# Kernel tuning notes

Hardware: AMD Instinct MI355X
Metric: run time of the kernel (lower is better)

The kernel has to match this reference:

```python
import jax, jax.numpy as jnp
import numpy as np

EPS = 1e-5
NUM_HEADS = 8


def _conv(x, w, pad, dil=1, groups=1, b=None):
    y = jax.lax.conv_general_dilated(
        x, w, (1, 1), pad, rhs_dilation=(dil, dil),
        dimension_numbers=('NCHW', 'OIHW', 'NCHW'), feature_group_count=groups)
    if b is not None:
        y = y + b[None, :, None, None]
    return y


def _bn_relu(x, gamma, beta):
    # BatchNorm2d in training mode: batch statistics over (N,H,W) per channel
    mu = x.mean(axis=(0, 2, 3), keepdims=True)
    var = x.var(axis=(0, 2, 3), keepdims=True)
    y = (x - mu) / jnp.sqrt(var + EPS) * gamma[None, :, None, None] + beta[None, :, None, None]
    return jax.nn.relu(y)


def _ln(x, w, b):
    # WithBias LayerNorm over channel dim (to_3d makes C the last axis)
    mu = x.mean(axis=1, keepdims=True)
    var = x.var(axis=1, keepdims=True)
    return (x - mu) / jnp.sqrt(var + EPS) * w[None, :, None, None] + b[None, :, None, None]


def _l2n(t):
    # torch F.normalize: x / max(||x||_2, 1e-12)
    return t / jnp.maximum(jnp.linalg.norm(t, axis=-1, keepdims=True), 1e-12)


def _forward(x, ln_w, ln_b, wd1, gd1, bd1, wd2, gd2, bd2, wd3, gd3, bd3,
             w_out1, w1, b1, w2, b2, w3, b3, w4, b4, w5, b5, w6, b6, w_out2):
    B, C, H, W = x.shape
    head, ch = NUM_HEADS, C // NUM_HEADS
    x1 = _ln(x, ln_w, ln_b)
    # dilated dense-conv branch (DConv2d = conv -> BN -> ReLU), dilations [1,6,12]
    x11 = _bn_relu(_conv(x, wd1, ((0, 0), (0, 0))), gd1, bd1)
    x12 = _bn_relu(_conv(x, wd2, ((6, 6), (6, 6)), dil=6), gd2, bd2)
    x13 = _bn_relu(_conv(x, wd3, ((12, 12), (12, 12)), dil=12), gd3, bd3)
    out2 = _conv(x11 + x12 + x13, w_out1, ((0, 0), (0, 0))) + x
    # six depthwise conv branches, summed
    att = (_conv(x1, w1, ((0, 0), (2, 2)), groups=C, b=b1)
           + _conv(x1, w2, ((2, 2), (0, 0)), groups=C, b=b2)
           + _conv(x1, w3, ((0, 0), (0, 0)), groups=C, b=b3)
           + _conv(x1, w4, ((1, 1), (1, 1)), groups=C, b=b4)
           + _conv(x1, w5, ((0, 0), (3, 3)), groups=C, b=b5)
           + _conv(x1, w6, ((3, 3), (0, 0)), groups=C, b=b6))
    out1 = _conv(att, w_out2, ((0, 0), (0, 0)))

    def r_hwc(t):  # b (head c) h w -> b head h (w c)
        return t.reshape(B, head, ch, H, W).transpose(0, 1, 3, 4, 2).reshape(B, head, H, W * ch)

    def r_whc(t):  # b (head c) h w -> b head w (h c)
        return t.reshape(B, head, ch, H, W).transpose(0, 1, 4, 3, 2).reshape(B, head, W, H * ch)

    k1 = _l2n(r_hwc(out1))
    v1 = r_hwc(out1)
    k2 = _l2n(r_whc(out2))
    v2 = r_whc(out2)
    q2 = _l2n(r_whc(out1))
    q1 = _l2n(r_whc(out2))
    A1 = jax.nn.softmax(q1 @ jnp.swapaxes(k1, -2, -1), axis=-1)  # [B,head,W,H]
    out3 = A1 @ v1 + q1
    A2 = jax.nn.softmax(q2 @ jnp.swapaxes(k2, -2, -1), axis=-1)
    out4 = A2 @ v2 + q2
    # b head h (w c) -> b (head c) h w
    o3 = out3.reshape(B, head, H, W, ch).transpose(0, 1, 4, 2, 3).reshape(B, C, H, W)
    # b head w (h c) -> b (head c) h w
    o4 = out4.reshape(B, head, W, H, ch).transpose(0, 1, 4, 3, 2).reshape(B, C, H, W)
    return _conv(o3, w_out2, ((0, 0), (0, 0))) + _conv(o4, w_out2, ((0, 0), (0, 0))) + x


def setup_inputs() -> dict:
    key = jax.random.key(0)
    ks = jax.random.split(key, 16)
    B, C, H, W = 8, 128, 128, 128

    def rn(k, shape, s):
        return jax.random.normal(k, shape, jnp.float32) * s

    inp = {}
    inp['x'] = jax.random.normal(ks[0], (B, C, H, W), jnp.float32)
    inp['ln_w'] = jnp.ones((C,), jnp.float32)
    inp['ln_b'] = jnp.zeros((C,), jnp.float32)
    inp['wd1'] = rn(ks[1], (C, C, 1, 1), 0.1)
    inp['gd1'] = jnp.ones((C,), jnp.float32)
    inp['bd1'] = jnp.zeros((C,), jnp.float32)
    inp['wd2'] = rn(ks[2], (C, C, 3, 3), 0.04)
    inp['gd2'] = jnp.ones((C,), jnp.float32)
    inp['bd2'] = jnp.zeros((C,), jnp.float32)
    inp['wd3'] = rn(ks[3], (C, C, 3, 3), 0.04)
    inp['gd3'] = jnp.ones((C,), jnp.float32)
    inp['bd3'] = jnp.zeros((C,), jnp.float32)
    inp['w_out1'] = rn(ks[4], (C, C, 1, 1), 0.09)
    inp['w1'] = rn(ks[5], (C, 1, 1, 5), 0.3)
    inp['b1'] = jnp.zeros((C,), jnp.float32)
    inp['w2'] = rn(ks[6], (C, 1, 5, 1), 0.3)
    inp['b2'] = jnp.zeros((C,), jnp.float32)
    inp['w3'] = rn(ks[7], (C, 1, 1, 1), 0.5)
    inp['b3'] = jnp.zeros((C,), jnp.float32)
    inp['w4'] = rn(ks[8], (C, 1, 3, 3), 0.2)
    inp['b4'] = jnp.zeros((C,), jnp.float32)
    inp['w5'] = rn(ks[9], (C, 1, 1, 7), 0.25)
    inp['b5'] = jnp.zeros((C,), jnp.float32)
    inp['w6'] = rn(ks[10], (C, 1, 7, 1), 0.25)
    inp['b6'] = jnp.zeros((C,), jnp.float32)
    inp['w_out2'] = rn(ks[11], (C, C, 1, 1), 0.09)
    return inp


def reference(x, ln_w, ln_b, wd1, gd1, bd1, wd2, gd2, bd2, wd3, gd3, bd3,
              w_out1, w1, b1, w2, b2, w3, b3, w4, b4, w5, b5, w6, b6, w_out2):
    return _forward(x, ln_w, ln_b, wd1, gd1, bd1, wd2, gd2, bd2, wd3, gd3, bd3,
                    w_out1, w1, b1, w2, b2, w3, b3, w4, b4, w5, b5, w6, b6, w_out2)
```

## Files before the change

kernel.cpp:

```cpp
#include <hip/hip_runtime.h>

#define Bb 8
#define Cc 128
#define Hh 128
#define Ww 128
#define HW 16384
#define CHW (Cc*HW)
#define NHW (Bb*HW)
#define CH 16
#define EPS 1e-5f

typedef __attribute__((ext_vector_type(8))) short bf16x8;
typedef __attribute__((ext_vector_type(4))) float f32x4;

static __device__ __forceinline__ short f2b(float f) {
  unsigned u = __float_as_uint(f);
  unsigned lsb = (u >> 16) & 1;
  return (short)((u + 0x7fffu + lsb) >> 16);
}
static __device__ __forceinline__ float b2f(short s) {
  return __uint_as_float(((unsigned)(unsigned short)s) << 16);
}

__global__ __launch_bounds__(256) void k_ln(const float* __restrict__ x,
    const float* __restrict__ g, const float* __restrict__ be,
    float* __restrict__ y)
{
  int p = blockIdx.x*256 + threadIdx.x;
  int b = p >> 14, hw = p & 16383;
  const float* xp = x + (long)b*CHW + hw;
  float s = 0.f, q = 0.f;
  for (int c = 0; c < Cc; ++c) { float v = xp[c*HW]; s += v; q += v*v; }
  float mu = s * (1.f/Cc);
  float var = q * (1.f/Cc) - mu*mu;
  float rstd = rsqrtf(var + EPS);
  float* yp = y + (long)b*CHW + hw;
  for (int c = 0; c < Cc; ++c) {
    float v = xp[c*HW];
    yp[c*HW] = (v - mu) * rstd * g[c] + be[c];
  }
}

__global__ __launch_bounds__(256) void k_reorg3b(const float* __restrict__ Wt, short* __restrict__ out)
{
  int idx = blockIdx.x*256 + threadIdx.x;
  int tap = idx >> 14, r = idx & 16383;
  out[idx] = f2b(Wt[r*9 + tap]);
}

__global__ __launch_bounds__(256) void k_cast(const float* __restrict__ in, short* __restrict__ out)
{
  int i = blockIdx.x*256 + threadIdx.x;
  out[i] = f2b(in[i]);
}

__global__ __launch_bounds__(256) void k_zero(float* p, int n)
{
  int i = blockIdx.x*256 + threadIdx.x;
  if (i < n) p[i] = 0.f;
}

__global__ __launch_bounds__(256) void k_nhwc(const float* __restrict__ in, short* __restrict__ out)
{
  __shared__ float Ls[32][33];
  int bid = blockIdx.x;
  int hwt = bid & 511, c4 = (bid>>9)&3, b = bid>>11;
  int hw0 = hwt << 5, c0 = c4 << 5;
  int t = threadIdx.x;
  int hl = t & 31, cl = t >> 5;
  const float* p = in + (long)b*CHW + hw0;
  for (int r = cl; r < 32; r += 8)
    Ls[r][hl] = p[(long)(c0+r)*HW + hl];
  __syncthreads();
  short* q = out + ((long)b*HW + hw0)*Cc + c0;
  int ccl = t & 31, hl0 = t >> 5;
  for (int r = hl0; r < 32; r += 8)
    q[(long)r*Cc + ccl] = f2b(Ls[ccl][r]);
}

__global__ __launch_bounds__(256,2) void k_mconv(const short* __restrict__ X,
    const short* __restrict__ W, float* __restrict__ Y, int k3, int dil)
{
  __shared__ short Ws[128*136];
  __shared__ short Xs[152*136];
  int b = blockIdx.x >> 7, h = blockIdx.x & 127;
  int t = threadIdx.x;
  int wave = t >> 6, lane = t & 63;
  int co0 = (wave >> 1) << 6, sp0 = (wave & 1) << 6;
  int lm = lane & 15, quad = lane >> 4;
  f32x4 acc[4][4];
  #pragma unroll
  for (int i = 0; i < 4; ++i)
    #pragma unroll
    for (int j = 0; j < 4; ++j) acc[i][j] = (f32x4){0.f,0.f,0.f,0.f};
  int half = k3 >> 1;

  {
    f32x4 z = {0.f,0.f,0.f,0.f};
    for (int i = t; i < 408; i += 256) {
      int r = i / 17, o = i - r*17;
      int row = r < 12 ? r : r + 128;
      *(f32x4*)(Xs + row*136 + o*8) = z;
    }
  }

  for (int kh = 0; kh < k3; ++kh) {
    int hs = h + (kh - half)*dil;
    if ((unsigned)hs >= (unsigned)Hh) continue;
    __syncthreads();
    {
      const short* xr = X + ((long)(b*Hh + hs)*Ww)*Cc;
      #pragma unroll
      for (int it = 0; it < 8; ++it) {
        int i = t + it*256;
        int row = i >> 4, off = (i & 15) << 3;
        *(f32x4*)(Xs + (12 + row)*136 + off) = *(const f32x4*)(xr + (long)row*Cc + off);
      }
    }
    for (int kw = 0; kw < k3; ++kw) {
      int dw = (kw - half)*dil;
      if (kw) __syncthreads();
      {
        const short* wt = W + (kh*k3 + kw)*16384;
        #pragma unroll
        for (int it = 0; it < 8; ++it) {
          int i = t + it*256;
          int row = i >> 4, off = (i & 15) << 3;
          *(f32x4*)(Ws + row*136 + off) = *(const f32x4*)(wt + (long)row*128 + off);
        }
      }
      __syncthreads();
      int xrow0 = 12 + dw + sp0;
      for (int kc = 0; kc < 4; ++kc) {
        int k0 = kc << 5;
        bf16x8 af[4], bfr[4];
        #pragma unroll
        for (int i = 0; i < 4; ++i)
          af[i] = *(const bf16x8*)(Ws + (co0 + i*16 + lm)*136 + k0 + quad*8);
        #pragma unroll
        for (int j = 0; j < 4; ++j)
          bfr[j] = *(const bf16x8*)(Xs + (xrow0 + j*16 + lm)*136 + k0 + quad*8);
        #pragma unroll
        for (int i = 0; i < 4; ++i)
          #pragma unroll
          for (int j = 0; j < 4; ++j)
            acc[i][j] = __builtin_amdgcn_mfma_f32_16x16x32_bf16(af[i], bfr[j], acc[i][j], 0, 0, 0);
      }
    }
  }
  float* yb = Y + ((long)(b*Hh + h)*Ww)*Cc;
  #pragma unroll
  for (int i = 0; i < 4; ++i) {
    int co = co0 + i*16 + quad*4;
    #pragma unroll
    for (int j = 0; j < 4; ++j) {
      int wc = sp0 + j*16 + lm;
      *(f32x4*)(yb + (long)wc*Cc + co) = acc[i][j];
    }
  }
}

__global__ __launch_bounds__(256,4) void k_mconv1(const short* __restrict__ X,
    const short* __restrict__ W, const float* __restrict__ res,
    float* __restrict__ Y, int nhwc)
{
  __shared__ short Ws[128*136];
  int b = blockIdx.x >> 7, h = blockIdx.x & 127;
  int t = threadIdx.x;
  int wave = t >> 6, lane = t & 63;
  int co0 = (wave >> 1) << 6, sp0 = (wave & 1) << 6;
  int lm = lane & 15, quad = lane >> 4;
  #pragma unroll
  for (int it = 0; it < 8; ++it) {
    int i = t + it*256;
    int row = i >> 4, off = (i & 15) << 3;
    *(f32x4*)(Ws + row*136 + off) = *(const f32x4*)(W + (long)row*128 + off);
  }
  f32x4 acc[4][4];
  #pragma unroll
  for (int i = 0; i < 4; ++i)
    #pragma unroll
    for (int j = 0; j < 4; ++j) acc[i][j] = (f32x4){0.f,0.f,0.f,0.f};
  const short* xr = X + ((long)(b*Hh + h)*Ww)*Cc;
  __syncthreads();
  #pragma unroll
  for (int kc = 0; kc < 4; ++kc) {
    int k0 = kc << 5;
    bf16x8 af[4], bfr[4];
    #pragma unroll
    for (int j = 0; j < 4; ++j)
      bfr[j] = *(const bf16x8*)(xr + (long)(sp0 + j*16 + lm)*Cc + k0 + quad*8);
    #pragma unroll
    for (int i = 0; i < 4; ++i)
      af[i] = *(const bf16x8*)(Ws + (co0 + i*16 + lm)*136 + k0 + quad*8);
    #pragma unroll
    for (int i = 0; i < 4; ++i)
      #pragma unroll
      for (int j = 0; j < 4; ++j)
        acc[i][j] = __builtin_amdgcn_mfma_f32_16x16x32_bf16(af[i], bfr[j], acc[i][j], 0, 0, 0);
  }
  if (nhwc) {
    float* yb = Y + ((long)(b*Hh + h)*Ww)*Cc;
    #pragma unroll
    for (int i = 0; i < 4; ++i) {
      int co = co0 + i*16 + quad*4;
      #pragma unroll
      for (int j = 0; j < 4; ++j) {
        int wc = sp0 + j*16 + lm;
        *(f32x4*)(yb + (long)wc*Cc + co) = acc[i][j];
      }
    }
  } else {
    __syncthreads();
    float* scr = (float*)Ws + wave*320;
    int co_l = lane >> 2, wq = (lane & 3) << 2;
    #pragma unroll
    for (int i = 0; i < 4; ++i) {
      #pragma unroll
      for (int j = 0; j < 4; ++j) {
        #pragma unroll
        for (int r = 0; r < 4; ++r)
          scr[(quad*4 + r)*20 + lm] = acc[i][j][r];
        f32x4 vv = *(f32x4*)(scr + co_l*20 + wq);
        int co = co0 + i*16 + co_l;
        int wc = sp0 + j*16 + wq;
        long idx = ((long)(b*Cc + co)*Hh + h)*Ww + wc;
        if (res) vv += *(const f32x4*)(res + idx);
        *(f32x4*)(Y + idx) = vv;
      }
    }
  }
}

__global__ __launch_bounds__(256) void k_bnstats(const float* __restrict__ y1,
    const float* __restrict__ y2, const float* __restrict__ y3,
    float* __restrict__ stats)
{
  __shared__ f32x4 Ls[8][32], Lq[8][32];
  int bid = blockIdx.x;
  int pt = bid & 31, b = (bid >> 5) & 7, tsel = bid >> 8;
  const float* y = tsel == 0 ? y1 : (tsel == 1 ? y2 : y3);
  const f32x4* p4 = (const f32x4*)(y + ((long)b*HW + pt*512)*Cc);
  int t = threadIdx.x;
  int cg = t & 31, pr = t >> 5;
  f32x4 s = {0.f,0.f,0.f,0.f}, q = {0.f,0.f,0.f,0.f};
  for (int k = 0; k < 64; ++k) {
    f32x4 v = p4[(long)(pr + k*8)*32 + cg];
    s += v; q += v*v;
  }
  Ls[pr][cg] = s; Lq[pr][cg] = q;
  __syncthreads();
  if (t < 32) {
    f32x4 ts = {0.f,0.f,0.f,0.f}, tq = {0.f,0.f,0.f,0.f};
    #pragma unroll
    for (int r = 0; r < 8; ++r) { ts += Ls[r][t]; tq += Lq[r][t]; }
    #pragma unroll
    for (int e = 0; e < 4; ++e) {
      atomicAdd(&stats[tsel*256 + t*4 + e], ts[e]);
      atomicAdd(&stats[tsel*256 + 128 + t*4 + e], tq[e]);
    }
  }
}

__global__ __launch_bounds__(128) void k_bnfin(const float* __restrict__ stats,
    const float* __restrict__ g1, const float* __restrict__ be1,
    const float* __restrict__ g2, const float* __restrict__ be2,
    const float* __restrict__ g3, const float* __restrict__ be3,
    float* __restrict__ so)
{
  int c = threadIdx.x;
  const float inv = 1.f/(float)NHW;
  const float* gs[3] = {g1, g2, g3};
  const float* bs[3] = {be1, be2, be3};
  #pragma unroll
  for (int tsel = 0; tsel < 3; ++tsel) {
    float mu = stats[tsel*256 + c]*inv;
    float var = stats[tsel*256 + 128 + c]*inv - mu*mu;
    float s = rsqrtf(var + EPS)*gs[tsel][c];
    so[tsel*256 + c] = s;
    so[tsel*256 + 128 + c] = bs[tsel][c] - mu*s;
  }
}

__global__ __launch_bounds__(256) void k_bnapply(const float* __restrict__ y1,
    const float* __restrict__ y2, const float* __restrict__ y3,
    const float* __restrict__ so, short* __restrict__ sb)
{
  long e = ((long)blockIdx.x*256 + threadIdx.x) * 8;
  int c = (int)(e & 127);
  f32x4 s1a = *(const f32x4*)(so + c),        s1b = *(const f32x4*)(so + c + 4);
  f32x4 o1a = *(const f32x4*)(so + 128 + c),  o1b = *(const f32x4*)(so + 132 + c);
  f32x4 s2a = *(const f32x4*)(so + 256 + c),  s2b = *(const f32x4*)(so + 260 + c);
  f32x4 o2a = *(const f32x4*)(so + 384 + c),  o2b = *(const f32x4*)(so + 388 + c);
  f32x4 s3a = *(const f32x4*)(so + 512 + c),  s3b = *(const f32x4*)(so + 516 + c);
  f32x4 o3a = *(const f32x4*)(so + 640 + c),  o3b = *(const f32x4*)(so + 644 + c);
  f32x4 v1a = *(const f32x4*)(y1 + e), v1b = *(const f32x4*)(y1 + e + 4);
  f32x4 v2a = *(const f32x4*)(y2 + e), v2b = *(const f32x4*)(y2 + e + 4);
  f32x4 v3a = *(const f32x4*)(y3 + e), v3b = *(const f32x4*)(y3 + e + 4);
  float r[8];
  #pragma unroll
  for (int k = 0; k < 4; ++k) {
    r[k] = fmaxf(fmaf(v1a[k], s1a[k], o1a[k]), 0.f)
         + fmaxf(fmaf(v2a[k], s2a[k], o2a[k]), 0.f)
         + fmaxf(fmaf(v3a[k], s3a[k], o3a[k]), 0.f);
    r[4+k] = fmaxf(fmaf(v1b[k], s1b[k], o1b[k]), 0.f)
           + fmaxf(fmaf(v2b[k], s2b[k], o2b[k]), 0.f)
           + fmaxf(fmaf(v3b[k], s3b[k], o3b[k]), 0.f);
  }
  int4 o;
  o.x = ((int)(unsigned short)f2b(r[1])<<16) | (unsigned short)f2b(r[0]);
  o.y = ((int)(unsigned short)f2b(r[3])<<16) | (unsigned short)f2b(r[2]);
  o.z = ((int)(unsigned short)f2b(r[5])<<16) | (unsigned short)f2b(r[4]);
  o.w = ((int)(unsigned short)f2b(r[7])<<16) | (unsigned short)f2b(r[6]);
  *(int4*)(sb + e) = o;
}

__global__ __launch_bounds__(256) void k_dw2(const float* __restrict__ X,
    const float* __restrict__ w1, const float* __restrict__ b1,
    const float* __restrict__ w2, const float* __restrict__ b2,
    const float* __restrict__ w3, const float* __restrict__ b3,
    const float* __restrict__ w4, const float* __restrict__ b4,
    const float* __restrict__ w5, const float* __restrict__ b5,
    const float* __restrict__ w6, const float* __restrict__ b6,
    float* __restrict__ Y)
{
  __shared__ float Ls[38][136];
  int bid = blockIdx.x;
  int tile = bid & 3, plane = bid >> 2;
  int c = plane & 127;
  int h0 = tile << 5;
  int t = threadIdx.x;

  float hcoef[7], vcoef[7], k9[9];
  #pragma unroll
  for (int d = 0; d < 7; ++d) { hcoef[d] = w5[c*7+d]; vcoef[d] = w6[c*7+d]; }
  #pragma unroll
  for (int d = 1; d < 6; ++d) { hcoef[d] += w1[c*5+d-1]; vcoef[d] += w2[c*5+d-1]; }
  hcoef[3] += w3[c];
  #pragma unroll
  for (int k = 0; k < 9; ++k) k9[k] = w4[c*9+k];
  float bias = b1[c]+b2[c]+b3[c]+b4[c]+b5[c]+b6[c];

  const float* xp = X + (long)plane*HW;

  f32x4* lz = (f32x4*)&Ls[0][0];
  for (int i = t; i < 1292; i += 256) lz[i] = (f32x4){0.f,0.f,0.f,0.f};
  __syncthreads();
  for (int i = t; i < 1216; i += 256) {
    int r = i >> 5, cg = (i & 31) << 2;
    int h = h0 - 3 + r;
    if ((unsigned)h < 128u)
      *(f32x4*)&Ls[r][4 + cg] = *(const f32x4*)(xp + h*128 + cg);
  }
  __syncthreads();

  int g = t & 31, rs = t >> 5;
  int w0 = g << 2;
  float* Yp = Y + (long)plane*HW;

  for (int ro = 0; ro < 4; ++ro) {
    int lr = rs + (ro << 3);
    int R = lr + 3;
    f32x4 a0 = *(const f32x4*)&Ls[R][w0];
    f32x4 a1 = *(const f32x4*)&Ls[R][w0+4];
    f32x4 a2 = *(const f32x4*)&Ls[R][w0+8];
    f32x4 u0 = *(const f32x4*)&Ls[R-1][w0];
    f32x4 u1 = *(const f32x4*)&Ls[R-1][w0+4];
    f32x4 u2 = *(const f32x4*)&Ls[R-1][w0+8];
    f32x4 d0 = *(const f32x4*)&Ls[R+1][w0];
    f32x4 d1 = *(const f32x4*)&Ls[R+1][w0+4];
    f32x4 d2 = *(const f32x4*)&Ls[R+1][w0+8];
    f32x4 v3u = *(const f32x4*)&Ls[R-3][w0+4];
    f32x4 v2u = *(const f32x4*)&Ls[R-2][w0+4];
    f32x4 v2d = *(const f32x4*)&Ls[R+2][w0+4];
    f32x4 v3d = *(const f32x4*)&Ls[R+3][w0+4];

    float cr[12], ur[12], dr[12];
    #pragma unroll
    for (int k = 0; k < 4; ++k) {
      cr[k] = a0[k]; cr[4+k] = a1[k]; cr[8+k] = a2[k];
      ur[k] = u0[k]; ur[4+k] = u1[k]; ur[8+k] = u2[k];
      dr[k] = d0[k]; dr[4+k] = d1[k]; dr[8+k] = d2[k];
    }

    f32x4 o;
    #pragma unroll
    for (int j = 0; j < 4; ++j) {
      float acc = bias;
      #pragma unroll
      for (int d = 0; d < 7; ++d) acc = fmaf(hcoef[d], cr[j+d+1], acc);
      acc = fmaf(vcoef[0], v3u[j], acc);
      acc = fmaf(vcoef[1], v2u[j], acc);
      acc = fmaf(vcoef[2], ur[j+4], acc);
      acc = fmaf(vcoef[3], cr[j+4], acc);
      acc = fmaf(vcoef[4], dr[j+4], acc);
      acc = fmaf(vcoef[5], v2d[j], acc);
      acc = fmaf(vcoef[6], v3d[j], acc);
      #pragma unroll
      for (int kw = 0; kw < 3; ++kw) {
        acc = fmaf(k9[kw],   ur[j+3+kw], acc);
        acc = fmaf(k9[3+kw], cr[j+3+kw], acc);
        acc = fmaf(k9[6+kw], dr[j+3+kw], acc);
      }
      o[j] = acc;
    }
    *(f32x4*)(Yp + (h0 + lr)*128 + w0) = o;
  }
}

__global__ __launch_bounds__(256) void k_normh(const float* __restrict__ out1, float* __restrict__ invn)
{
  __shared__ float red[256];
  int bid = blockIdx.x;
  int h = bid & 127; int bh = bid >> 7;
  int b = bh >> 3, hd = bh & 7;
  const float* p = out1 + ((long)(b*Cc + hd*CH)*Hh + h)*Ww;
  float s = 0.f;
  for (int e = threadIdx.x; e < 2048; e += 256) {
    int c = e >> 7, w = e & 127;
    float v = p[(long)c*HW + w];
    s += v*v;
  }
  red[threadIdx.x] = s; __syncthreads();
  for (int st = 128; st > 0; st >>= 1) {
    if (threadIdx.x < st) red[threadIdx.x] += red[threadIdx.x+st];
    __syncthreads();
  }
  if (threadIdx.x == 0) invn[bid] = 1.f/fmaxf(sqrtf(red[0]), 1e-12f);
}

__global__ __launch_bounds__(256) void k_normw_part(const float* __restrict__ out1,
    const float* __restrict__ out2, float* __restrict__ acc1, float* __restrict__ acc2)
{
  __shared__ float red[4][256];
  int bid = blockIdx.x;
  int c = bid & 15, bh = (bid >> 4) & 63, tsel = bid >> 10;
  int b = bh >> 3, hd = bh & 7;
  const float* p = (tsel ? out2 : out1) + (long)(b*Cc + hd*CH + c)*HW;
  int t = threadIdx.x;
  const float4* p4 = (const float4*)p;
  float s0 = 0.f, s1 = 0.f, s2 = 0.f, s3 = 0.f;
  for (int i = t; i < 4096; i += 256) {
    float4 v = p4[i];
    s0 += v.x*v.x; s1 += v.y*v.y; s2 += v.z*v.z; s3 += v.w*v.w;
  }
  red[0][t] = s0; red[1][t] = s1; red[2][t] = s2; red[3][t] = s3;
  __syncthreads();
  if (t < 128) {
    int j = t >> 5;
    int g = t & 31;
    float tot = 0.f;
    #pragma unroll
    for (int r = 0; r < 8; ++r) tot += red[j][g + r*32];
    atomicAdd((tsel ? acc2 : acc1) + bh*128 + g*4 + j, tot);
  }
}

__global__ __launch_bounds__(256) void k_finw(float* __restrict__ p)
{
  int i = blockIdx.x*256 + threadIdx.x;
  float v = p[i];
  p[i] = 1.f/fmaxf(sqrtf(v), 1e-12f);
}

__global__ __launch_bounds__(256) void k_t12(const float* __restrict__ out1,
    const float* __restrict__ out2, short* __restrict__ out1T, short* __restrict__ out2T)
{
  __shared__ float Ls[32][33];
  int bid = blockIdx.x;
  int wt = bid&3, ht=(bid>>2)&3, c=(bid>>4)&127, b=(bid>>11)&7, src=bid>>14;
  const float* in = (src ? out2 : out1) + (long)(b*128+c)*16384;
  short* outp = (src ? out2T : out1T) + ((long)(b*8 + (c>>4))*128)*2048 + (c&15)*128;
  int h0 = ht*32, w0 = wt*32;
  int t = threadIdx.x, li = t&31, r0 = t>>5;
  for (int r = r0; r < 32; r += 8)
    Ls[r][li] = in[(h0+r)*128 + w0 + li];
  __syncthreads();
  for (int r = r0; r < 32; r += 8)
    outp[(long)(w0+r)*2048 + h0 + li] = f2b(Ls[li][r]);
}

__global__ __launch_bounds__(256) void k_h12(const float* __restrict__ out1,
    const float* __restrict__ out2, short* __restrict__ out1H, short* __restrict__ out2H)
{
  int bid = blockIdx.x;
  int src = bid >> 13;
  long e = ((long)(bid & 8191)*256 + threadIdx.x) * 8;
  const float* p;
  short* dst;
  if (src) { p = out2 + e; dst = out2H + e; }
  else {
    int c = (int)((e>>7)&15), h = (int)((e>>11)&127), hd=(int)((e>>18)&7), b=(int)(e>>21);
    int pp = (int)(e & 127);
    p = out1 + (((long)(b*128 + hd*16 + c)*128 + h)*128 + pp);
    dst = out1H + e;
  }
  int4 o;
  o.x = ((int)(unsigned short)f2b(p[1])<<16) | (unsigned short)f2b(p[0]);
  o.y = ((int)(unsigned short)f2b(p[3])<<16) | (unsigned short)f2b(p[2]);
  o.z = ((int)(unsigned short)f2b(p[5])<<16) | (unsigned short)f2b(p[4]);
  o.w = ((int)(unsigned short)f2b(p[7])<<16) | (unsigned short)f2b(p[6]);
  *(int4*)dst = o;
}

__global__ __launch_bounds__(256) void k_attnS_m(
    const short* __restrict__ out1T, const short* __restrict__ out2T,
    const short* __restrict__ out1H,
    const float* __restrict__ invn1h, const float* __restrict__ invn1w,
    const float* __restrict__ invn2w,
    short* __restrict__ A1b, short* __restrict__ A2b)
{
  __shared__ short As[128*72];
  __shared__ short Bs[128*72];
  int bid = blockIdx.x;
  int type = bid >> 6, bh = bid & 63;
  const short* Aop = (type ? out1T : out2T) + (long)bh*262144;
  const short* Bop = (type ? out2T : out1H) + (long)bh*262144;
  const float* invrow = (type ? invn1w : invn2w) + bh*128;
  const float* invcol = (type ? invn2w : invn1h) + bh*128;
  short* Aout = (type ? A2b : A1b) + (long)bh*16384;
  int t = threadIdx.x;
  int wave = t >> 6, lane = t & 63, lm = lane & 15, quad = lane >> 4;
  int m0 = wave << 5;
  f32x4 acc[2][8];
  #pragma unroll
  for (int i = 0; i < 2; ++i)
    #pragma unroll
    for (int j = 0; j < 8; ++j) acc[i][j] = (f32x4){0.f,0.f,0.f,0.f};
  for (int kc = 0; kc < 32; ++kc) {
    int k0 = kc << 6;
    __syncthreads();
    #pragma unroll
    for (int i = 0; i < 4; ++i) {
      int e = t + i*256;
      int row = e >> 3, off = (e & 7) << 3;
      *(float4*)(As + row*72 + off) = *(const float4*)(Aop + (long)row*2048 + k0 + off);
      *(float4*)(Bs + row*72 + off) = *(const float4*)(Bop + (long)row*2048 + k0 + off);
    }
    __syncthreads();
    #pragma unroll
    for (int ks = 0; ks < 64; ks += 32) {
      bf16x8 af[2], bfj[8];
      #pragma unroll
      for (int i = 0; i < 2; ++i)
        af[i] = *(const bf16x8*)(As + (m0 + i*16 + lm)*72 + ks + quad*8);
      #pragma unroll
      for (int j = 0; j < 8; ++j)
        bfj[j] = *(const bf16x8*)(Bs + (j*16 + lm)*72 + ks + quad*8);
      #pragma unroll
      for (int i = 0; i < 2; ++i)
        #pragma unroll
        for (int j = 0; j < 8; ++j)
          acc[i][j] = __builtin_amdgcn_mfma_f32_16x16x32_bf16(af[i], bfj[j], acc[i][j], 0, 0, 0);
    }
  }
  float colv[8];
  #pragma unroll
  for (int j = 0; j < 8; ++j) colv[j] = invcol[j*16 + lm];
  #pragma unroll
  for (int i = 0; i < 2; ++i) {
    #pragma unroll
    for (int r = 0; r < 4; ++r) {
      int row = m0 + i*16 + quad*4 + r;
      float rs = invrow[row];
      float sv[8];
      float mx = -1e30f;
      #pragma unroll
      for (int j = 0; j < 8; ++j) {
        sv[j] = acc[i][j][r] * rs * colv[j];
        mx = fmaxf(mx, sv[j]);
      }
      mx = fmaxf(mx, __shfl_xor(mx, 1));
      mx = fmaxf(mx, __shfl_xor(mx, 2));
      mx = fmaxf(mx, __shfl_xor(mx, 4));
      mx = fmaxf(mx, __shfl_xor(mx, 8));
      float sum = 0.f;
      #pragma unroll
      for (int j = 0; j < 8; ++j) { sv[j] = __expf(sv[j] - mx); sum += sv[j]; }
      sum += __shfl_xor(sum, 1);
      sum += __shfl_xor(sum, 2);
      sum += __shfl_xor(sum, 4);
      sum += __shfl_xor(sum, 8);
      float inv = 1.f/sum;
      #pragma unroll
      for (int j = 0; j < 8; ++j)
        Aout[row*128 + j*16 + lm] = f2b(sv[j]*inv);
    }
  }
}

__global__ __launch_bounds__(256) void k_o34m(
    const short* __restrict__ A1b, const short* __restrict__ out1T,
    const short* __restrict__ out1H, const float* __restrict__ invn1w,
    const short* __restrict__ out2H, const short* __restrict__ A2b,
    float* __restrict__ o34, int mode)
{
  __shared__ short As[128*72];
  __shared__ short Bs[128*72];
  int bid = blockIdx.x;
  const short *Abase, *Bbase;
  long Astride, Bstride;
  float* O;
  const short* R = nullptr;
  const float* inw = nullptr;
  if (mode == 0) {
    int c = bid & 15, hd = (bid>>4)&7, b = bid>>7;
    int bh = b*8+hd;
    Abase = A1b + (long)bh*16384; Astride = 128;
    Bbase = out1T + (long)bh*262144 + c*128; Bstride = 2048;
    O = o34 + (long)(b*128 + hd*16 + c)*16384;
    R = out1H + (long)bh*262144 + c*128;
    inw = invn1w + bh*128;
  } else {
    int cf = bid & 127, b = bid >> 7;
    int bh = b*8 + (cf>>4);
    Abase = out2H + (long)(b*128+cf)*16384; Astride = 128;
    Bbase = A2b + (long)bh*16384; Bstride = 128;
    O = o34 + (long)(b*128+cf)*16384;
  }
  int t = threadIdx.x;
  int wave = t >> 6, lane = t & 63, lm = lane & 15, quad = lane >> 4;
  int m0 = (wave >> 1) << 6, n0 = (wave & 1) << 6;
  f32x4 acc[4][4];
  #pragma unroll
  for (int i = 0; i < 4; ++i)
    #pragma unroll
    for (int j = 0; j < 4; ++j) acc[i][j] = (f32x4){0.f,0.f,0.f,0.f};
  for (int kc = 0; kc < 2; ++kc) {
    int k0 = kc << 6;
    __syncthreads();
    #pragma unroll
    for (int i = 0; i < 4; ++i) {
      int e = t + i*256;
      int row = e >> 3, off = (e & 7) << 3;
      *(float4*)(As + row*72 + off) = *(const float4*)(Abase + (long)row*Astride + k0 + off);
      *(float4*)(Bs + row*72 + off) = *(const float4*)(Bbase + (long)row*Bstride + k0 + off);
    }
    __syncthreads();
    #pragma unroll
    for (int ks = 0; ks < 64; ks += 32) {
      bf16x8 af[4], bfj[4];
      #pragma unroll
      for (int i = 0; i < 4; ++i)
        af[i] = *(const bf16x8*)(As + (m0 + i*16 + lm)*72 + ks + quad*8);
      #pragma unroll
      for (int j = 0; j < 4; ++j)
        bfj[j] = *(const bf16x8*)(Bs + (n0 + j*16 + lm)*72 + ks + quad*8);
      #pragma unroll
      for (int i = 0; i < 4; ++i)
        #pragma unroll
        for (int j = 0; j < 4; ++j)
          acc[i][j] = __builtin_amdgcn_mfma_f32_16x16x32_bf16(af[i], bfj[j], acc[i][j], 0, 0, 0);
    }
  }
  if (mode == 0) {
    float inwv[4];
    #pragma unroll
    for (int j = 0; j < 4; ++j) inwv[j] = inw[n0 + j*16 + lm];
    #pragma unroll
    for (int i = 0; i < 4; ++i) {
      #pragma unroll
      for (int r = 0; r < 4; ++r) {
        int row = m0 + i*16 + quad*4 + r;
        #pragma unroll
        for (int j = 0; j < 4; ++j) {
          int col = n0 + j*16 + lm;
          float rv = b2f(R[(long)row*2048 + col]);
          O[row*128 + col] = acc[i][j][r] + rv * inwv[j];
        }
      }
    }
  } else {
    #pragma unroll
    for (int i = 0; i < 4; ++i) {
      #pragma unroll
      for (int r = 0; r < 4; ++r) {
        int row = m0 + i*16 + quad*4 + r;
        #pragma unroll
        for (int j = 0; j < 4; ++j) {
          int col = n0 + j*16 + lm;
          O[row*128 + col] += acc[i][j][r];
        }
      }
    }
  }
}

__global__ __launch_bounds__(256) void k_tadd(const float* __restrict__ out2,
    const float* __restrict__ invn2w, float* o34)
{
  __shared__ float Ls[32][33];
  int bid = blockIdx.x;
  int wi = bid & 3, hi = (bid>>2)&3, cc = (bid>>4)&127, b = bid>>11;
  int h0 = hi*32, w0 = wi*32;
  int hd = cc >> 4;
  int t = threadIdx.x;
  int li = t & 31, r0 = t >> 5;
  const float* p = out2 + (long)(b*Cc+cc)*HW;
  for (int r = r0; r < 32; r += 8)
    Ls[r][li] = p[(w0+r)*128 + h0 + li];
  __syncthreads();
  float* q = o34 + (long)(b*Cc+cc)*HW;
  for (int r = r0; r < 32; r += 8) {
    float iv = invn2w[(((b<<3)+hd)<<7) + h0 + r];
    q[(h0+r)*128 + w0 + li] += Ls[li][r] * iv;
  }
}

extern "C" void kernel_launch(void* const* d_in, const int* in_sizes, int n_in,
                              void* d_out, int out_size, void* d_ws, size_t ws_size,
                              hipStream_t stream)
{
  const float* x    = (const float*)d_in[0];
  const float* ln_w = (const float*)d_in[1];
  const float* ln_b = (const float*)d_in[2];
  const float* wd1  = (const float*)d_in[3];
  const float* gd1  = (const float*)d_in[4];
  const float* bd1  = (const float*)d_in[5];
  const float* wd2  = (const float*)d_in[6];
  const float* gd2  = (const float*)d_in[7];
  const float* bd2  = (const float*)d_in[8];
  const float* wd3  = (const float*)d_in[9];
  const float* gd3  = (const float*)d_in[10];
  const float* bd3  = (const float*)d_in[11];
  const float* w_out1 = (const float*)d_in[12];
  const float* w1 = (const float*)d_in[13]; const float* b1 = (const float*)d_in[14];
  const float* w2 = (const float*)d_in[15]; const float* b2 = (const float*)d_in[16];
  const float* w3 = (const float*)d_in[17]; const float* b3 = (const float*)d_in[18];
  const float* w4 = (const float*)d_in[19]; const float* b4 = (const float*)d_in[20];
  const float* w5 = (const float*)d_in[21]; const float* b5 = (const float*)d_in[22];
  const float* w6 = (const float*)d_in[23]; const float* b6 = (const float*)d_in[24];
  const float* w_out2 = (const float*)d_in[25];
  float* out = (float*)d_out;

  const long SLAB = 16777216L;
  float* buf0 = (float*)d_ws;
  float* buf1 = buf0 + SLAB;
  float* buf2 = buf1 + SLAB;
  float* dbuf = out;
  float* stats = buf2 + SLAB;
  float* invn1h = stats + 768;
  float* invn1w = invn1h + 8192;
  float* invn2w = invn1w + 8192;
  short* wb2  = (short*)(invn2w + 8192);
  short* wb3  = wb2 + 147456;
  short* wb1  = wb3 + 147456;
  short* wbo1 = wb1 + 16384;
  short* wbo2 = wbo1 + 16384;
  short* A1b  = wbo2 + 16384;
  short* A2b  = A1b + 1048576;
  float* bnso = (float*)(A2b + 1048576);

  short* xb = (short*)buf0;
  short* sb = (short*)buf0;
  short* ab = (short*)buf1;
  short* out1T = (short*)dbuf;
  short* out2T = out1T + 16777216;
  short* out1H = (short*)buf1;
  short* out2H = out1H + 16777216;
  short* ob = (short*)buf1;

  k_zero<<<3, 256, 0, stream>>>(stats, 768);
  k_zero<<<64, 256, 0, stream>>>(invn1w, 16384);
  k_reorg3b<<<576, 256, 0, stream>>>(wd2, wb2);
  k_reorg3b<<<576, 256, 0, stream>>>(wd3, wb3);
  k_cast<<<64, 256, 0, stream>>>(wd1, wb1);
  k_cast<<<64, 256, 0, stream>>>(w_out1, wbo1);
  k_cast<<<64, 256, 0, stream>>>(w_out2, wbo2);

  k_nhwc<<<16384, 256, 0, stream>>>(x, xb);
  k_mconv1<<<1024, 256, 0, stream>>>(xb, wb1, nullptr, buf1, 1);
  k_mconv<<<1024, 256, 0, stream>>>(xb, wb2, buf2, 3, 6);
  k_mconv<<<1024, 256, 0, stream>>>(xb, wb3, dbuf, 3, 12);
  k_bnstats<<<768, 256, 0, stream>>>(buf1, buf2, dbuf, stats);
  k_bnfin<<<1, 128, 0, stream>>>(stats, gd1, bd1, gd2, bd2, gd3, bd3, bnso);
  k_bnapply<<<8192, 256, 0, stream>>>(buf1, buf2, dbuf, bnso, sb);
  k_mconv1<<<1024, 256, 0, stream>>>(sb, wbo1, x, buf2, 0);
  k_ln<<<512, 256, 0, stream>>>(x, ln_w, ln_b, buf0);
  k_dw2<<<4096, 256, 0, stream>>>(buf0, w1,b1,w2,b2,w3,b3,w4,b4,w5,b5,w6,b6, dbuf);
  k_nhwc<<<16384, 256, 0, stream>>>(dbuf, ab);
  k_mconv1<<<1024, 256, 0, stream>>>(ab, wbo2, nullptr, buf0, 0);
  k_normh<<<8192, 256, 0, stream>>>(buf0, invn1h);
  k_normw_part<<<2048, 256, 0, stream>>>(buf0, buf2, invn1w, invn2w);
  k_finw<<<64, 256, 0, stream>>>(invn1w);
  k_t12<<<32768, 256, 0, stream>>>(buf0, buf2, out1T, out2T);
  k_h12<<<16384, 256, 0, stream>>>(buf0, buf2, out1H, out2H);
  k_attnS_m<<<128, 256, 0, stream>>>(out1T, out2T, out1H,
                                     invn1h, invn1w, invn2w, A1b, A2b);
  k_o34m<<<1024, 256, 0, stream>>>(A1b, out1T, out1H, invn1w,
                                   out2H, A2b, buf0, 0);
  k_o34m<<<1024, 256, 0, stream>>>(A1b, out1T, out1H, invn1w,
                                   out2H, A2b, buf0, 1);
  k_tadd<<<16384, 256, 0, stream>>>(buf2, invn2w, buf0);
  k_nhwc<<<16384, 256, 0, stream>>>(buf0, ob);
  k_mconv1<<<1024, 256, 0, stream>>>(ob, wbo2, x, out, 0);
}
```

Before: 840.1 us.

## Fuse BN statistics into conv epilogues and merge o34 GEMMs with transpose-add

Batch-norm sum and sum-of-squares are now accumulated in the epilogues of the three dilated-conv kernels through wave shuffles and atomics, so the separate stats pass that re-read three large fp32 tensors is gone. The two o34 GEMM launches and the transpose-add kernel become a single kernel. It accumulates both products in registers, adds the residual terms, and writes each output once through an LDS-staged coalesced store instead of doing read-modify-write passes. The cost is more atomics, with per-block contention on 256 addresses, and a heavier epilogue with strided reads of out2.

```diff
diff --git a/kernel.cpp b/kernel.cpp
--- a/kernel.cpp
+++ b/kernel.cpp
@@ -20,6 +20,33 @@
 }
 static __device__ __forceinline__ float b2f(short s) {
   return __uint_as_float(((unsigned)(unsigned short)s) << 16);
+}
+
+static __device__ __forceinline__ void stats_epilogue(
+    float* __restrict__ statp, f32x4 acc[4][4], int co0, int quad, int lm)
+{
+  #pragma unroll
+  for (int i = 0; i < 4; ++i) {
+    f32x4 s = acc[i][0] + acc[i][1] + acc[i][2] + acc[i][3];
+    f32x4 q = acc[i][0]*acc[i][0] + acc[i][1]*acc[i][1]
+            + acc[i][2]*acc[i][2] + acc[i][3]*acc[i][3];
+    #pragma unroll
+    for (int m = 1; m < 16; m <<= 1) {
+      #pragma unroll
+      for (int e = 0; e < 4; ++e) {
+        s[e] += __shfl_xor(s[e], m);
+        q[e] += __shfl_xor(q[e], m);
+      }
+    }
+    if (lm == 0) {
+      int co = co0 + i*16 + quad*4;
+      #pragma unroll
+      for (int e = 0; e < 4; ++e) {
+        atomicAdd(&statp[co + e], s[e]);
+        atomicAdd(&statp[128 + co + e], q[e]);
+      }
+    }
+  }
 }
 
 __global__ __launch_bounds__(256) void k_ln(const float* __restrict__ x,
@@ -79,7 +106,8 @@
 }
 
 __global__ __launch_bounds__(256,2) void k_mconv(const short* __restrict__ X,
-    const short* __restrict__ W, float* __restrict__ Y, int k3, int dil)
+    const short* __restrict__ W, float* __restrict__ Y, int k3, int dil,
+    float* __restrict__ statp)
 {
   __shared__ short Ws[128*136];
   __shared__ short Xs[152*136];
@@ -158,11 +186,12 @@
       *(f32x4*)(yb + (long)wc*Cc + co) = acc[i][j];
     }
   }
+  if (statp) stats_epilogue(statp, acc, co0, quad, lm);
 }
 
 __global__ __launch_bounds__(256,4) void k_mconv1(const short* __restrict__ X,
     const short* __restrict__ W, const float* __restrict__ res,
-    float* __restrict__ Y, int nhwc)
+    float* __restrict__ Y, int nhwc, float* __restrict__ statp)
 {
   __shared__ short Ws[128*136];
   int b = blockIdx.x >> 7, h = blockIdx.x & 127;
@@ -210,6 +239,7 @@
         *(f32x4*)(yb + (long)wc*Cc + co) = acc[i][j];
       }
     }
+    if (statp) stats_epilogue(statp, acc, co0, quad, lm);
   } else {
     __syncthreads();
     float* scr = (float*)Ws + wave*320;
@@ -228,36 +258,6 @@
         if (res) vv += *(const f32x4*)(res + idx);
         *(f32x4*)(Y + idx) = vv;
       }
-    }
-  }
-}
-
-__global__ __launch_bounds__(256) void k_bnstats(const float* __restrict__ y1,
-    const float* __restrict__ y2, const float* __restrict__ y3,
-    float* __restrict__ stats)
-{
-  __shared__ f32x4 Ls[8][32], Lq[8][32];
-  int bid = blockIdx.x;
-  int pt = bid & 31, b = (bid >> 5) & 7, tsel = bid >> 8;
-  const float* y = tsel == 0 ? y1 : (tsel == 1 ? y2 : y3);
-  const f32x4* p4 = (const f32x4*)(y + ((long)b*HW + pt*512)*Cc);
-  int t = threadIdx.x;
-  int cg = t & 31, pr = t >> 5;
-  f32x4 s = {0.f,0.f,0.f,0.f}, q = {0.f,0.f,0.f,0.f};
-  for (int k = 0; k < 64; ++k) {
-    f32x4 v = p4[(long)(pr + k*8)*32 + cg];
-    s += v; q += v*v;
-  }
-  Ls[pr][cg] = s; Lq[pr][cg] = q;
-  __syncthreads();
-  if (t < 32) {
-    f32x4 ts = {0.f,0.f,0.f,0.f}, tq = {0.f,0.f,0.f,0.f};
-    #pragma unroll
-    for (int r = 0; r < 8; ++r) { ts += Ls[r][t]; tq += Lq[r][t]; }
-    #pragma unroll
-    for (int e = 0; e < 4; ++e) {
-      atomicAdd(&stats[tsel*256 + t*4 + e], ts[e]);
-      atomicAdd(&stats[tsel*256 + 128 + t*4 + e], tq[e]);
     }
   }
 }
@@ -589,35 +589,28 @@
   }
 }
 
-__global__ __launch_bounds__(256) void k_o34m(
+__global__ __launch_bounds__(256) void k_o34f(
     const short* __restrict__ A1b, const short* __restrict__ out1T,
     const short* __restrict__ out1H, const float* __restrict__ invn1w,
     const short* __restrict__ out2H, const short* __restrict__ A2b,
-    float* __restrict__ o34, int mode)
+    const float* __restrict__ out2, const float* __restrict__ invn2w,
+    float* __restrict__ o34)
 {
   __shared__ short As[128*72];
   __shared__ short Bs[128*72];
   int bid = blockIdx.x;
-  const short *Abase, *Bbase;
-  long Astride, Bstride;
-  float* O;
-  const short* R = nullptr;
-  const float* inw = nullptr;
-  if (mode == 0) {
-    int c = bid & 15, hd = (bid>>4)&7, b = bid>>7;
-    int bh = b*8+hd;
-    Abase = A1b + (long)bh*16384; Astride = 128;
-    Bbase = out1T + (long)bh*262144 + c*128; Bstride = 2048;
-    O = o34 + (long)(b*128 + hd*16 + c)*16384;
-    R = out1H + (long)bh*262144 + c*128;
-    inw = invn1w + bh*128;
-  } else {
-    int cf = bid & 127, b = bid >> 7;
-    int bh = b*8 + (cf>>4);
-    Abase = out2H + (long)(b*128+cf)*16384; Astride = 128;
-    Bbase = A2b + (long)bh*16384; Bstride = 128;
-    O = o34 + (long)(b*128+cf)*16384;
-  }
+  int cf = bid & 127, b = bid >> 7;
+  int hd = cf >> 4, c = cf & 15;
+  int bh = b*8 + hd;
+  const short* A0 = A1b + (long)bh*16384;
+  const short* B0 = out1T + (long)bh*262144 + c*128;
+  const short* A1_ = out2H + (long)(b*128 + cf)*16384;
+  const short* B1_ = A2b + (long)bh*16384;
+  const short* R = out1H + (long)bh*262144 + c*128;
+  const float* o2p = out2 + (long)(b*128 + cf)*16384;
+  const float* inw1 = invn1w + bh*128;
+  const float* inw2 = invn2w + bh*128;
+  float* O = o34 + (long)(b*128 + cf)*16384;
   int t = threadIdx.x;
   int wave = t >> 6, lane = t & 63, lm = lane & 15, quad = lane >> 4;
   int m0 = (wave >> 1) << 6, n0 = (wave & 1) << 6;
@@ -626,15 +619,18 @@
   for (int i = 0; i < 4; ++i)
     #pragma unroll
     for (int j = 0; j < 4; ++j) acc[i][j] = (f32x4){0.f,0.f,0.f,0.f};
-  for (int kc = 0; kc < 2; ++kc) {
-    int k0 = kc << 6;
+  for (int g = 0; g < 4; ++g) {
+    const short* Asrc = (g < 2) ? A0 : A1_;
+    const short* Bsrc = (g < 2) ? B0 : B1_;
+    long Bst = (g < 2) ? 2048 : 128;
+    int k0 = (g & 1) << 6;
     __syncthreads();
     #pragma unroll
     for (int i = 0; i < 4; ++i) {
       int e = t + i*256;
       int row = e >> 3, off = (e & 7) << 3;
-      *(float4*)(As + row*72 + off) = *(const float4*)(Abase + (long)row*Astride + k0 + off);
-      *(float4*)(Bs + row*72 + off) = *(const float4*)(Bbase + (long)row*Bstride + k0 + off);
+      *(float4*)(As + row*72 + off) = *(const float4*)(Asrc + (long)row*128 + k0 + off);
+      *(float4*)(Bs + row*72 + off) = *(const float4*)(Bsrc + (long)row*Bst + k0 + off);
     }
     __syncthreads();
     #pragma unroll
@@ -653,57 +649,36 @@
           acc[i][j] = __builtin_amdgcn_mfma_f32_16x16x32_bf16(af[i], bfj[j], acc[i][j], 0, 0, 0);
     }
   }
-  if (mode == 0) {
-    float inwv[4];
-    #pragma unroll
-    for (int j = 0; j < 4; ++j) inwv[j] = inw[n0 + j*16 + lm];
-    #pragma unroll
-    for (int i = 0; i < 4; ++i) {
-      #pragma unroll
-      for (int r = 0; r < 4; ++r) {
-        int row = m0 + i*16 + quad*4 + r;
-        #pragma unroll
-        for (int j = 0; j < 4; ++j) {
-          int col = n0 + j*16 + lm;
-          float rv = b2f(R[(long)row*2048 + col]);
-          O[row*128 + col] = acc[i][j][r] + rv * inwv[j];
-        }
-      }
-    }
-  } else {
-    #pragma unroll
-    for (int i = 0; i < 4; ++i) {
-      #pragma unroll
-      for (int r = 0; r < 4; ++r) {
-        int row = m0 + i*16 + quad*4 + r;
-        #pragma unroll
-        for (int j = 0; j < 4; ++j) {
-          int col = n0 + j*16 + lm;
-          O[row*128 + col] += acc[i][j][r];
-        }
-      }
-    }
-  }
-}
-
-__global__ __launch_bounds__(256) void k_tadd(const float* __restrict__ out2,
-    const float* __restrict__ invn2w, float* o34)
-{
-  __shared__ float Ls[32][33];
-  int bid = blockIdx.x;
-  int wi = bid & 3, hi = (bid>>2)&3, cc = (bid>>4)&127, b = bid>>11;
-  int h0 = hi*32, w0 = wi*32;
-  int hd = cc >> 4;
-  int t = threadIdx.x;
-  int li = t & 31, r0 = t >> 5;
-  const float* p = out2 + (long)(b*Cc+cc)*HW;
-  for (int r = r0; r < 32; r += 8)
-    Ls[r][li] = p[(w0+r)*128 + h0 + li];
+  float inwv[4];
+  #pragma unroll
+  for (int j = 0; j < 4; ++j) inwv[j] = inw1[n0 + j*16 + lm];
+  #pragma unroll
+  for (int i = 0; i < 4; ++i) {
+    int row0 = m0 + i*16 + quad*4;
+    f32x4 iv2 = *(const f32x4*)(inw2 + row0);
+    #pragma unroll
+    for (int j = 0; j < 4; ++j) {
+      int col = n0 + j*16 + lm;
+      f32x4 vq = *(const f32x4*)(o2p + (long)col*128 + row0);
+      #pragma unroll
+      for (int r = 0; r < 4; ++r)
+        acc[i][j][r] += b2f(R[(long)(row0 + r)*2048 + col]) * inwv[j]
+                      + vq[r] * iv2[r];
+    }
+  }
   __syncthreads();
-  float* q = o34 + (long)(b*Cc+cc)*HW;
-  for (int r = r0; r < 32; r += 8) {
-    float iv = invn2w[(((b<<3)+hd)<<7) + h0 + r];
-    q[(h0+r)*128 + w0 + li] += Ls[li][r] * iv;
+  float* scr = (float*)As + wave*320;
+  int co_l = lane >> 2, wq = (lane & 3) << 2;
+  #pragma unroll
+  for (int i = 0; i < 4; ++i) {
+    #pragma unroll
+    for (int j = 0; j < 4; ++j) {
+      #pragma unroll
+      for (int r = 0; r < 4; ++r)
+        scr[(quad*4 + r)*20 + lm] = acc[i][j][r];
+      f32x4 vv = *(f32x4*)(scr + co_l*20 + wq);
+      *(f32x4*)(O + (long)(m0 + i*16 + co_l)*128 + n0 + j*16 + wq) = vv;
+    }
   }
 }
 
@@ -769,17 +744,16 @@
   k_cast<<<64, 256, 0, stream>>>(w_out2, wbo2);
 
   k_nhwc<<<16384, 256, 0, stream>>>(x, xb);
-  k_mconv1<<<1024, 256, 0, stream>>>(xb, wb1, nullptr, buf1, 1);
-  k_mconv<<<1024, 256, 0, stream>>>(xb, wb2, buf2, 3, 6);
-  k_mconv<<<1024, 256, 0, stream>>>(xb, wb3, dbuf, 3, 12);
-  k_bnstats<<<768, 256, 0, stream>>>(buf1, buf2, dbuf, stats);
+  k_mconv1<<<1024, 256, 0, stream>>>(xb, wb1, nullptr, buf1, 1, stats);
+  k_mconv<<<1024, 256, 0, stream>>>(xb, wb2, buf2, 3, 6, stats + 256);
+  k_mconv<<<1024, 256, 0, stream>>>(xb, wb3, dbuf, 3, 12, stats + 512);
   k_bnfin<<<1, 128, 0, stream>>>(stats, gd1, bd1, gd2, bd2, gd3, bd3, bnso);
   k_bnapply<<<8192, 256, 0, stream>>>(buf1, buf2, dbuf, bnso, sb);
-  k_mconv1<<<1024, 256, 0, stream>>>(sb, wbo1, x, buf2, 0);
+  k_mconv1<<<1024, 256, 0, stream>>>(sb, wbo1, x, buf2, 0, nullptr);
   k_ln<<<512, 256, 0, stream>>>(x, ln_w, ln_b, buf0);
   k_dw2<<<4096, 256, 0, stream>>>(buf0, w1,b1,w2,b2,w3,b3,w4,b4,w5,b5,w6,b6, dbuf);
   k_nhwc<<<16384, 256, 0, stream>>>(dbuf, ab);
-  k_mconv1<<<1024, 256, 0, stream>>>(ab, wbo2, nullptr, buf0, 0);
+  k_mconv1<<<1024, 256, 0, stream>>>(ab, wbo2, nullptr, buf0, 0, nullptr);
   k_normh<<<8192, 256, 0, stream>>>(buf0, invn1h);
   k_normw_part<<<2048, 256, 0, stream>>>(buf0, buf2, invn1w, invn2w);
   k_finw<<<64, 256, 0, stream>>>(invn1w);
@@ -787,11 +761,8 @@
   k_h12<<<16384, 256, 0, stream>>>(buf0, buf2, out1H, out2H);
   k_attnS_m<<<128, 256, 0, stream>>>(out1T, out2T, out1H,
                                      invn1h, invn1w, invn2w, A1b, A2b);
-  k_o34m<<<1024, 256, 0, stream>>>(A1b, out1T, out1H, invn1w,
-                                   out2H, A2b, buf0, 0);
-  k_o34m<<<1024, 256, 0, stream>>>(A1b, out1T, out1H, invn1w,
-                                   out2H, A2b, buf0, 1);
-  k_tadd<<<16384, 256, 0, stream>>>(buf2, invn2w, buf0);
+  k_o34f<<<1024, 256, 0, stream>>>(A1b, out1T, out1H, invn1w,
+                                   out2H, A2b, buf2, invn2w, buf0);
   k_nhwc<<<16384, 256, 0, stream>>>(buf0, ob);
-  k_mconv1<<<1024, 256, 0, stream>>>(ob, wbo2, x, out, 0);
-}
+  k_mconv1<<<1024, 256, 0, stream>>>(ob, wbo2, x, out, 0, nullptr);
+}
```

Result: slower. 1.280 ms (+52.4%).
